# Optimization experiments

Hardware: AMD Instinct MI355X
Metric: run time of the kernel (lower is better)

Reference implementation:

```python
import jax, jax.numpy as jnp
import numpy as np

D_MODEL = 2048
NUM_HEADS = 16
HEAD_DIM = D_MODEL // NUM_HEADS


def setup_inputs() -> dict:
    key = jax.random.key(0)
    ks = jax.random.split(key, 11)
    B, S = 2, 2048
    s = 1.0 / np.sqrt(D_MODEL)
    return {
        "query": jax.random.normal(ks[0], (B, S, D_MODEL), jnp.float32),
        "key_in": jax.random.normal(ks[1], (B, S, D_MODEL), jnp.float32),
        "value": jax.random.normal(ks[2], (B, S, D_MODEL), jnp.float32),
        "Wq": jax.random.normal(ks[3], (D_MODEL, D_MODEL), jnp.float32) * s,
        "bq": jnp.zeros((D_MODEL,), jnp.float32),
        "Wk": jax.random.normal(ks[4], (D_MODEL, D_MODEL), jnp.float32) * s,
        "bk": jnp.zeros((D_MODEL,), jnp.float32),
        "Wv": jax.random.normal(ks[5], (D_MODEL, D_MODEL), jnp.float32) * s,
        "bv": jnp.zeros((D_MODEL,), jnp.float32),
        "Wo": jax.random.normal(ks[6], (D_MODEL, D_MODEL), jnp.float32) * s,
        "bo": jnp.zeros((D_MODEL,), jnp.float32),
    }


def reference(query, key_in, value, Wq, bq, Wk, bk, Wv, bv, Wo, bo):
    B, S, _ = query.shape
    # projections (torch Linear: x @ W.T + b)
    q = query @ Wq.T + bq
    k = key_in @ Wk.T + bk
    v = value @ Wv.T + bv
    # [B, H, S, Dh]
    q = q.reshape(B, S, NUM_HEADS, HEAD_DIM).transpose(0, 2, 1, 3)
    k = k.reshape(B, -1, NUM_HEADS, HEAD_DIM).transpose(0, 2, 1, 3)
    v = v.reshape(B, -1, NUM_HEADS, HEAD_DIM).transpose(0, 2, 1, 3)
    scores = jnp.einsum("bhqd,bhkd->bhqk", q, k) / np.sqrt(HEAD_DIM).astype(np.float32)
    attn = jax.nn.softmax(scores, axis=-1)
    out = jnp.einsum("bhqk,bhkd->bhqd", attn, v)
    out = out.transpose(0, 2, 1, 3).reshape(B, S, D_MODEL)
    return out @ Wo.T + bo
```

## Files before the change

### kernel.cpp

```cpp
#include <hip/hip_runtime.h>
#include <hip/hip_bf16.h>
#include <stdint.h>

typedef __hip_bfloat16 bf16;
typedef __attribute__((ext_vector_type(8))) short bf16x8;
typedef __attribute__((ext_vector_type(4))) float f32x4;
typedef __attribute__((ext_vector_type(4))) short s16x4;

constexpr int D_MODEL   = 2048;
constexpr int NUM_HEADS = 16;
constexpr int HEAD_DIM  = 128;
constexpr int BATCH     = 2;
constexpr int SEQ       = 2048;

constexpr int GBM = 256, GBN = 128, GBK = 64;
constexpr int G_ABUF = GBM * GBK;
constexpr int G_BBUF = GBN * GBK;
constexpr int G_BUF  = G_ABUF + G_BBUF;
constexpr int G_LDS  = 3 * G_BUF;

__device__ __forceinline__ void gload_lds16(const bf16* g, bf16* l) {
    __builtin_amdgcn_global_load_lds(
        (const __attribute__((address_space(1))) void*)g,
        (__attribute__((address_space(3))) void*)l, 16, 0, 0);
}

struct CvtArgs { const float* src[7]; bf16* dst[7]; int n8[7]; };

__global__ __launch_bounds__(256)
void cvt_multi(CvtArgs a)
{
    const int t = blockIdx.y;
    const float* __restrict__ s = a.src[t];
    bf16* __restrict__ d = a.dst[t];
    const int n8 = a.n8[t];
    for (int i = blockIdx.x * 256 + threadIdx.x; i < n8; i += gridDim.x * 256) {
        f32x4 x = *(const f32x4*)(s + (size_t)i * 8);
        f32x4 y = *(const f32x4*)(s + (size_t)i * 8 + 4);
        bf16 t8[8] = { __float2bfloat16(x[0]), __float2bfloat16(x[1]),
                       __float2bfloat16(x[2]), __float2bfloat16(x[3]),
                       __float2bfloat16(y[0]), __float2bfloat16(y[1]),
                       __float2bfloat16(y[2]), __float2bfloat16(y[3]) };
        *(bf16x8*)(d + (size_t)i * 8) = *(const bf16x8*)t8;
    }
}

template <int P>
__device__ __forceinline__
void phase_mfma(f32x4 (&acc)[4][4], bf16x8 (&a)[4][2], bf16x8 (&b)[4][2])
{
#pragma unroll
    for (int kk = 0; kk < 2; kk++) {
#pragma unroll
        for (int j = 0; j <= P; j++)
            acc[P][j] = __builtin_amdgcn_mfma_f32_16x16x32_bf16(a[P][kk], b[j][kk], acc[P][j], 0, 0, 0);
#pragma unroll
        for (int i = 0; i < P; i++)
            acc[i][P] = __builtin_amdgcn_mfma_f32_16x16x32_bf16(a[i][kk], b[P][kk], acc[i][P], 0, 0, 0);
    }
}

template <typename TC, bool TRANS_PERM>
__device__ __forceinline__
void gemm_body(const bf16* __restrict__ A, const bf16* __restrict__ W,
               const float* __restrict__ bias, TC* __restrict__ C,
               int M, int N, int K, bf16* smem)
{
    const int tid  = threadIdx.x;
    const int lane = tid & 63;
    const int wave = tid >> 6;
    const int quad = lane >> 4, l16 = lane & 15;
    const int sw   = l16 & 7;
    const int wr   = wave >> 1;
    const int wc   = wave & 1;
    const int m0   = blockIdx.y * GBM, n0 = blockIdx.x * GBN;

    const int rloc = tid >> 3;
    const int gsw  = (tid & 7) ^ (rloc & 7);
    const int NT   = K / GBK;

    const bf16* Abase = A + (size_t)(m0 + rloc) * K + gsw * 8;
    const bf16* Bbase = W + (size_t)(n0 + rloc) * K + gsw * 8;
    const size_t rstep = (size_t)64 * K;

    auto stageA = [&](int t, int bi, int u) {
        gload_lds16(Abase + u * rstep + (size_t)t * GBK,
                    smem + bi * G_BUF + (u * 512 + tid) * 8);
    };
    auto stageB = [&](int t, int bi, int u) {
        gload_lds16(Bbase + u * rstep + (size_t)t * GBK,
                    smem + bi * G_BUF + G_ABUF + (u * 512 + tid) * 8);
    };

    f32x4 acc[4][4];
#pragma unroll
    for (int i = 0; i < 4; i++)
#pragma unroll
        for (int j = 0; j < 4; j++) acc[i][j] = (f32x4){0.f, 0.f, 0.f, 0.f};

    bf16x8 a[4][2], b[4][2];

#pragma unroll
    for (int u = 0; u < 4; u++) stageA(0, 0, u);
#pragma unroll
    for (int u = 0; u < 2; u++) stageB(0, 0, u);
    if (NT > 1) {
#pragma unroll
        for (int u = 0; u < 4; u++) stageA(1, 1, u);
#pragma unroll
        for (int u = 0; u < 2; u++) stageB(1, 1, u);
        asm volatile("s_waitcnt vmcnt(6)" ::: "memory");
    } else {
        asm volatile("s_waitcnt vmcnt(0)" ::: "memory");
    }
    asm volatile("s_barrier" ::: "memory");

#define GEMM_PHASE(p, STAGE_STMT)                                              \
    {                                                                          \
        STAGE_STMT;                                                            \
        const int rA = wr * 64 + (p) * 16 + l16;                               \
        const int rB = wc * 64 + (p) * 16 + l16;                               \
        a[p][0] = *(const bf16x8*)&sAc[rA * 64 + (quad ^ sw) * 8];             \
        a[p][1] = *(const bf16x8*)&sAc[rA * 64 + (((4 + quad) ^ sw)) * 8];     \
        b[p][0] = *(const bf16x8*)&sBc[rB * 64 + (quad ^ sw) * 8];             \
        b[p][1] = *(const bf16x8*)&sBc[rB * 64 + (((4 + quad) ^ sw)) * 8];     \
        __builtin_amdgcn_s_barrier();                                          \
        __builtin_amdgcn_s_setprio(1);                                         \
        phase_mfma<p>(acc, a, b);                                              \
        __builtin_amdgcn_s_setprio(0);                                         \
    }

    int bc = 0;
    for (int t = 0; t < NT; ++t) {
        const bf16* sAc = smem + bc * G_BUF;
        const bf16* sBc = sAc + G_ABUF;
        const int bs = (bc + 2 >= 3) ? bc - 1 : bc + 2;
        const bool pf = (t + 2 < NT);

        GEMM_PHASE(0, if (pf) { stageA(t + 2, bs, 0); stageA(t + 2, bs, 1); })
        __builtin_amdgcn_s_barrier();
        GEMM_PHASE(1, if (pf) { stageA(t + 2, bs, 2); stageA(t + 2, bs, 3); })
        __builtin_amdgcn_s_barrier();
        GEMM_PHASE(2, if (pf) { stageB(t + 2, bs, 0); })
        __builtin_amdgcn_s_barrier();
        GEMM_PHASE(3, if (pf) { stageB(t + 2, bs, 1); })
        if (pf)                asm volatile("s_waitcnt vmcnt(6)" ::: "memory");
        else if (t + 1 < NT)   asm volatile("s_waitcnt vmcnt(0)" ::: "memory");
        asm volatile("s_barrier" ::: "memory");
        bc = (bc + 1 == 3) ? 0 : bc + 1;
    }
#undef GEMM_PHASE

#pragma unroll
    for (int j = 0; j < 4; j++) {
        const int col = n0 + wc * 64 + j * 16 + l16;
        const float bv = bias[col];
#pragma unroll
        for (int i = 0; i < 4; i++) {
            const int row0 = m0 + wr * 64 + i * 16 + quad * 4;
            if constexpr (TRANS_PERM) {
                int g   = row0 & 63;
                int tau = g >> 4, qh = (g >> 2) & 3;
                int pp  = (tau >> 1) * 32 + qh * 8 + (tau & 1) * 4;
                int sp  = ((row0 & 2047) & ~63) | pp;
                size_t idx = (size_t)(row0 >> 11) * ((size_t)D_MODEL * SEQ)
                           + (size_t)col * SEQ + sp;
                bf16 t4[4];
#pragma unroll
                for (int r = 0; r < 4; r++) t4[r] = __float2bfloat16(acc[i][j][r] + bv);
                *(s16x4*)&C[idx] = *(const s16x4*)t4;
            } else {
#pragma unroll
                for (int r = 0; r < 4; r++) {
                    int row = row0 + r;
                    if constexpr (sizeof(TC) == 2)
                        C[(size_t)row * N + col] = (TC)__float2bfloat16(acc[i][j][r] + bv);
                    else
                        C[(size_t)row * N + col] = (TC)(acc[i][j][r] + bv);
                }
            }
        }
    }
}

template <typename TC, bool TRANS_PERM>
__global__ __launch_bounds__(512, 1)
void gemm_bf16(const bf16* __restrict__ A, const bf16* __restrict__ W,
               const float* __restrict__ bias, TC* __restrict__ C,
               int M, int N, int K)
{
    __shared__ bf16 smem[G_LDS];
    gemm_body<TC, TRANS_PERM>(A, W, bias, C, M, N, K, smem);
}

struct QkvArgs { const bf16* A[3]; const bf16* W[3]; const float* bias[3]; bf16* C[3]; };

__global__ __launch_bounds__(512, 1)
void gemm_qkv(QkvArgs ga, int M, int N, int K)
{
    __shared__ bf16 smem[G_LDS];
    const int z = blockIdx.z;
    if (z == 2) gemm_body<bf16, true >(ga.A[2], ga.W[2], ga.bias[2], ga.C[2], M, N, K, smem);
    else        gemm_body<bf16, false>(ga.A[z], ga.W[z], ga.bias[z], ga.C[z], M, N, K, smem);
}

struct QkArgs { const bf16* A[2]; const bf16* W[2]; const float* bias[2]; bf16* C[2]; };

__global__ __launch_bounds__(512, 1)
void gemm_qk(QkArgs ga, int M, int N, int K)
{
    __shared__ bf16 smem[G_LDS];
    const int z = blockIdx.z;
    gemm_body<bf16, false>(ga.A[z], ga.W[z], ga.bias[z], ga.C[z], M, N, K, smem);
}

__global__ __launch_bounds__(256)
void flash_attn_kernel(const bf16* __restrict__ Qp, const bf16* __restrict__ Kp,
                       const bf16* __restrict__ Vt, bf16* __restrict__ Op)
{
    constexpr int BQ = 128, BKV = 64, DH = 128;
    __shared__ bf16 sK[2][BKV * DH];
    __shared__ bf16 sV[2][DH * BKV];

    const int tid  = threadIdx.x;
    const int wave = tid >> 6, lane = tid & 63;
    const int quad = lane >> 4, l16 = lane & 15;
    const int q0 = blockIdx.x * BQ;
    const int h  = blockIdx.y;
    const int b  = blockIdx.z;

    const size_t base  = (size_t)b * SEQ * D_MODEL + (size_t)h * HEAD_DIM;
    const size_t basev = ((size_t)b * NUM_HEADS + h) * (size_t)HEAD_DIM * SEQ;
    const bf16* Kb = Kp + base;
    const bf16* Vb = Vt + basev;

    auto stage = [&](int t, int bi) {
        const bf16* Kt = Kb + (size_t)t * BKV * D_MODEL;
        const bf16* Vtile = Vb + (size_t)t * BKV;
        bf16* sKb = sK[bi];
        bf16* sVb = sV[bi];
#pragma unroll
        for (int s = 0; s < 4; s++) {
            int c = s * 256 + wave * 64 + lane;
            int row = c >> 4, gs = c & 15;
            int g = gs ^ (row & 15);
            gload_lds16(Kt + (size_t)row * D_MODEL + g * 8, sKb + (size_t)c * 8);
        }
#pragma unroll
        for (int s = 0; s < 4; s++) {
            int c = s * 256 + wave * 64 + lane;
            int dh = c >> 3, gs = c & 7;
            int g = gs ^ (dh & 7);
            gload_lds16(Vtile + (size_t)dh * SEQ + g * 8, sVb + (size_t)c * 8);
        }
    };

    bf16x8 bq[2][4];
#pragma unroll
    for (int nt = 0; nt < 2; nt++)
#pragma unroll
        for (int kk = 0; kk < 4; kk++)
            bq[nt][kk] = *(const bf16x8*)&Qp[base +
                (size_t)(q0 + wave * 32 + nt * 16 + l16) * D_MODEL + kk * 32 + quad * 8];

    f32x4 oacc[2][8];
#pragma unroll
    for (int nt = 0; nt < 2; nt++)
#pragma unroll
        for (int mt = 0; mt < 8; mt++) oacc[nt][mt] = (f32x4){0.f, 0.f, 0.f, 0.f};

    float lsum[2] = {0.f, 0.f};

    const float SCL2E = 0.08838834764831845f * 1.4426950408889634f;
    constexpr int NT = SEQ / BKV;

    stage(0, 0);

    for (int t = 0; t < NT; ++t) {
        __syncthreads();
        if (t + 1 < NT) stage(t + 1, (t + 1) & 1);

        const bf16* sKc = sK[t & 1];
        const bf16* sVc = sV[t & 1];

        f32x4 sacc[2][4];
#pragma unroll
        for (int nt = 0; nt < 2; nt++)
#pragma unroll
            for (int kt = 0; kt < 4; kt++) sacc[nt][kt] = (f32x4){0.f, 0.f, 0.f, 0.f};
#pragma unroll
        for (int kk = 0; kk < 4; kk++) {
            bf16x8 ak[4];
#pragma unroll
            for (int kt = 0; kt < 4; kt++) {
                int row = kt * 16 + l16;
                int g   = (kk * 4 + quad) ^ l16;
                ak[kt] = *(const bf16x8*)&sKc[(size_t)row * DH + g * 8];
            }
#pragma unroll
            for (int nt = 0; nt < 2; nt++)
#pragma unroll
                for (int kt = 0; kt < 4; kt++)
                    sacc[nt][kt] = __builtin_amdgcn_mfma_f32_16x16x32_bf16(ak[kt], bq[nt][kk], sacc[nt][kt], 0, 0, 0);
        }

        bf16x8 pb[2][2];
#pragma unroll
        for (int nt = 0; nt < 2; nt++) {
            bf16 tmp[16];
#pragma unroll
            for (int kt = 0; kt < 4; kt++) {
#pragma unroll
                for (int r = 0; r < 4; r++) {
                    float p = exp2f(fminf(sacc[nt][kt][r] * SCL2E, 60.f));
                    lsum[nt] += p;
                    tmp[(kt >> 1) * 8 + (kt & 1) * 4 + r] = __float2bfloat16(p);
                }
            }
            pb[nt][0] = *(const bf16x8*)&tmp[0];
            pb[nt][1] = *(const bf16x8*)&tmp[8];
        }

#pragma unroll
        for (int c = 0; c < 2; c++) {
#pragma unroll
            for (int mt = 0; mt < 8; mt++) {
                int row = mt * 16 + l16;
                int g   = (c * 4 + quad) ^ (l16 & 7);
                bf16x8 av = *(const bf16x8*)&sVc[(size_t)row * BKV + g * 8];
#pragma unroll
                for (int nt = 0; nt < 2; nt++)
                    oacc[nt][mt] = __builtin_amdgcn_mfma_f32_16x16x32_bf16(av, pb[nt][c], oacc[nt][mt], 0, 0, 0);
            }
        }
    }

#pragma unroll
    for (int nt = 0; nt < 2; nt++) {
        float v = lsum[nt];
        v += __shfl_xor(v, 16);
        v += __shfl_xor(v, 32);
        lsum[nt] = v;
    }

#pragma unroll
    for (int nt = 0; nt < 2; nt++) {
        float inv = 1.f / lsum[nt];
        int row = q0 + wave * 32 + nt * 16 + l16;
#pragma unroll
        for (int mt = 0; mt < 8; mt++) {
            bf16 t4[4];
#pragma unroll
            for (int r = 0; r < 4; r++) t4[r] = __float2bfloat16(oacc[nt][mt][r] * inv);
            *(s16x4*)&Op[base + (size_t)row * D_MODEL + mt * 16 + quad * 4] = *(const s16x4*)t4;
        }
    }
}

extern "C" void kernel_launch(void* const* d_in, const int* in_sizes, int n_in,
                              void* d_out, int out_size, void* d_ws, size_t ws_size,
                              hipStream_t stream)
{
    const float* query  = (const float*)d_in[0];
    const float* key_in = (const float*)d_in[1];
    const float* value  = (const float*)d_in[2];
    const float* Wq = (const float*)d_in[3];
    const float* bq = (const float*)d_in[4];
    const float* Wk = (const float*)d_in[5];
    const float* bk = (const float*)d_in[6];
    const float* Wv = (const float*)d_in[7];
    const float* bv = (const float*)d_in[8];
    const float* Wo = (const float*)d_in[9];
    const float* bo = (const float*)d_in[10];
    float* out = (float*)d_out;

    const int tokens = BATCH * SEQ;
    const size_t nAct = (size_t)tokens * D_MODEL;
    const size_t nW   = (size_t)D_MODEL * D_MODEL;

    const bool fused_qkv = ws_size >= (6 * nAct + 4 * nW) * sizeof(bf16);

    bf16* p = (bf16*)d_ws;
    bf16* qb  = p; p += nAct;
    bf16* kb  = p; p += nAct;
    bf16* vb  = p; p += nAct;
    bf16* wqb = p; p += nW;
    bf16* wkb = p; p += nW;
    bf16* wvb = p; p += nW;
    bf16* wob = p; p += nW;
    bf16* qp  = p; p += nAct;
    bf16* kp  = p; p += nAct;
    bf16* vpT;
    if (fused_qkv) { vpT = p; p += nAct; }
    else           { vpT = qb; }
    bf16* ap = fused_qkv ? qb : kb;

    CvtArgs ca;
    ca.src[0] = query;  ca.dst[0] = qb;  ca.n8[0] = (int)(nAct / 8);
    ca.src[1] = key_in; ca.dst[1] = kb;  ca.n8[1] = (int)(nAct / 8);
    ca.src[2] = value;  ca.dst[2] = vb;  ca.n8[2] = (int)(nAct / 8);
    ca.src[3] = Wq;     ca.dst[3] = wqb; ca.n8[3] = (int)(nW / 8);
    ca.src[4] = Wk;     ca.dst[4] = wkb; ca.n8[4] = (int)(nW / 8);
    ca.src[5] = Wv;     ca.dst[5] = wvb; ca.n8[5] = (int)(nW / 8);
    ca.src[6] = Wo;     ca.dst[6] = wob; ca.n8[6] = (int)(nW / 8);
    cvt_multi<<<dim3(512, 7), 256, 0, stream>>>(ca);

    if (fused_qkv) {
        QkvArgs qa;
        qa.A[0] = qb; qa.W[0] = wqb; qa.bias[0] = bq; qa.C[0] = qp;
        qa.A[1] = kb; qa.W[1] = wkb; qa.bias[1] = bk; qa.C[1] = kp;
        qa.A[2] = vb; qa.W[2] = wvb; qa.bias[2] = bv; qa.C[2] = vpT;
        dim3 g3(D_MODEL / 128, tokens / 256, 3);
        gemm_qkv<<<g3, 512, 0, stream>>>(qa, tokens, D_MODEL, D_MODEL);
    } else {
        QkArgs qa;
        qa.A[0] = qb; qa.W[0] = wqb; qa.bias[0] = bq; qa.C[0] = qp;
        qa.A[1] = kb; qa.W[1] = wkb; qa.bias[1] = bk; qa.C[1] = kp;
        dim3 g2(D_MODEL / 128, tokens / 256, 2);
        gemm_qk<<<g2, 512, 0, stream>>>(qa, tokens, D_MODEL, D_MODEL);
        dim3 gg(D_MODEL / 128, tokens / 256);
        gemm_bf16<bf16, true><<<gg, 512, 0, stream>>>(vb, wvb, bv, vpT, tokens, D_MODEL, D_MODEL);
    }

    dim3 ga(SEQ / 128, NUM_HEADS, BATCH);
    flash_attn_kernel<<<ga, 256, 0, stream>>>(qp, kp, vpT, ap);

    dim3 gg(D_MODEL / 128, tokens / 256);
    gemm_bf16<float, false><<<gg, 512, 0, stream>>>(ap, wob, bo, out, tokens, D_MODEL, D_MODEL);
}
```

Measured before the change: 488.6 us.

## Restructure GEMM main loop with double-buffered register fragments and inline-asm LDS reads

The GEMM inner loop is rewritten so that each K tile issues all its global-to-LDS prefetches at once. It then runs MFMAs on fragments held in registers while the next tile's fragments are read from LDS by a single inline-asm block of ds_read_b128 instructions. Register fragments are ping-ponged across a loop unrolled by two, and the per-phase barriers are removed, leaving one barrier per tile. Launch bounds are also raised to two blocks per CU, which constrains registers and may cause spills, and LDS use (about 144KB per block) may not allow a second block anyway.

```diff
diff --git a/kernel.cpp b/kernel.cpp
--- a/kernel.cpp
+++ b/kernel.cpp
@@ -24,6 +24,8 @@
         (const __attribute__((address_space(1))) void*)g,
         (__attribute__((address_space(3))) void*)l, 16, 0, 0);
 }
+
+typedef __attribute__((address_space(3))) const bf16 lds_cbf16;
 
 struct CvtArgs { const float* src[7]; bf16* dst[7]; int n8[7]; };
 
@@ -45,20 +47,67 @@
     }
 }
 
-template <int P>
-__device__ __forceinline__
-void phase_mfma(f32x4 (&acc)[4][4], bf16x8 (&a)[4][2], bf16x8 (&b)[4][2])
-{
-#pragma unroll
-    for (int kk = 0; kk < 2; kk++) {
-#pragma unroll
-        for (int j = 0; j <= P; j++)
-            acc[P][j] = __builtin_amdgcn_mfma_f32_16x16x32_bf16(a[P][kk], b[j][kk], acc[P][j], 0, 0, 0);
-#pragma unroll
-        for (int i = 0; i < P; i++)
-            acc[i][P] = __builtin_amdgcn_mfma_f32_16x16x32_bf16(a[i][kk], b[P][kk], acc[i][P], 0, 0, 0);
-    }
-}
+
+#define DS_READ16(A0, B0, A1, B1, vA0, vB0, vA1, vB1)                          \
+    asm volatile(                                                              \
+        "ds_read_b128 %0, %16 offset:0\n\t"                                    \
+        "ds_read_b128 %1, %16 offset:2048\n\t"                                 \
+        "ds_read_b128 %2, %16 offset:4096\n\t"                                 \
+        "ds_read_b128 %3, %16 offset:6144\n\t"                                 \
+        "ds_read_b128 %4, %17 offset:0\n\t"                                    \
+        "ds_read_b128 %5, %17 offset:2048\n\t"                                 \
+        "ds_read_b128 %6, %17 offset:4096\n\t"                                 \
+        "ds_read_b128 %7, %17 offset:6144\n\t"                                 \
+        "ds_read_b128 %8, %18 offset:0\n\t"                                    \
+        "ds_read_b128 %9, %18 offset:2048\n\t"                                 \
+        "ds_read_b128 %10, %18 offset:4096\n\t"                                \
+        "ds_read_b128 %11, %18 offset:6144\n\t"                                \
+        "ds_read_b128 %12, %19 offset:0\n\t"                                   \
+        "ds_read_b128 %13, %19 offset:2048\n\t"                                \
+        "ds_read_b128 %14, %19 offset:4096\n\t"                                \
+        "ds_read_b128 %15, %19 offset:6144"                                    \
+        : "=&v"(A0[0]), "=&v"(A0[1]), "=&v"(A0[2]), "=&v"(A0[3]),              \
+          "=&v"(B0[0]), "=&v"(B0[1]), "=&v"(B0[2]), "=&v"(B0[3]),              \
+          "=&v"(A1[0]), "=&v"(A1[1]), "=&v"(A1[2]), "=&v"(A1[3]),              \
+          "=&v"(B1[0]), "=&v"(B1[1]), "=&v"(B1[2]), "=&v"(B1[3])               \
+        : "v"(vA0), "v"(vB0), "v"(vA1), "v"(vB1))
+
+#define MFMA_HALF(AR, BR)                                                      \
+    {                                                                          \
+        __builtin_amdgcn_s_setprio(1);                                         \
+        _Pragma("unroll")                                                      \
+        for (int i_ = 0; i_ < 4; i_++)                                         \
+            _Pragma("unroll")                                                  \
+            for (int j_ = 0; j_ < 4; j_++)                                     \
+                acc[i_][j_] = __builtin_amdgcn_mfma_f32_16x16x32_bf16(         \
+                    AR[i_], BR[j_], acc[i_][j_], 0, 0, 0);                     \
+        __builtin_amdgcn_s_setprio(0);                                         \
+        __builtin_amdgcn_sched_barrier(0);                                     \
+    }
+
+#define GEMM_TILE(t, CA0, CB0, CA1, CB1, NA0, NB0, NA1, NB1)                   \
+    {                                                                          \
+        const int  bs_ = (bc + 2 >= 3) ? bc - 1 : bc + 2;                      \
+        const bool pf_ = (t) + 2 < NT;                                         \
+        if (pf_) { stageA((t) + 2, bs_, 0); stageA((t) + 2, bs_, 1);           \
+                   stageA((t) + 2, bs_, 2); stageA((t) + 2, bs_, 3);           \
+                   stageB((t) + 2, bs_, 0); stageB((t) + 2, bs_, 1); }         \
+        asm volatile("s_waitcnt lgkmcnt(0)" ::: "memory");    \
+        __builtin_amdgcn_sched_barrier(0);                                     \
+        MFMA_HALF(CA0, CB0);                                                   \
+        if (pf_)               asm volatile("s_waitcnt vmcnt(6)" ::: "memory");\
+        else if ((t) + 1 < NT) asm volatile("s_waitcnt vmcnt(0)" ::: "memory");\
+        asm volatile("s_barrier" ::: "memory");          \
+        if ((t) + 1 < NT) {                                                    \
+            const int bn_ = (bc + 1 >= 3) ? 0 : bc + 1;                        \
+            const uint32_t nA_ = aoffTh + (uint32_t)(bn_ * (G_BUF * 2));       \
+            const uint32_t nB_ = boffTh + (uint32_t)(bn_ * (G_BUF * 2));       \
+            DS_READ16(NA0, NB0, NA1, NB1, nA_, nB_, nA_ ^ 64u, nB_ ^ 64u);     \
+            __builtin_amdgcn_sched_barrier(0);        \
+        }                                                                      \
+        MFMA_HALF(CA1, CB1);                                                   \
+        bc = (bc + 1 == 3) ? 0 : bc + 1;                                       \
+    }
 
 template <typename TC, bool TRANS_PERM>
 __device__ __forceinline__
@@ -92,13 +141,19 @@
                     smem + bi * G_BUF + G_ABUF + (u * 512 + tid) * 8);
     };
 
+    const uint32_t aoffTh = (uint32_t)(uintptr_t)(lds_cbf16*)
+        &smem[(wr * 64 + l16) * 64 + (quad ^ sw) * 8];
+    const uint32_t boffTh = (uint32_t)(uintptr_t)(lds_cbf16*)
+        &smem[G_ABUF + (wc * 64 + l16) * 64 + (quad ^ sw) * 8];
+
     f32x4 acc[4][4];
 #pragma unroll
     for (int i = 0; i < 4; i++)
 #pragma unroll
         for (int j = 0; j < 4; j++) acc[i][j] = (f32x4){0.f, 0.f, 0.f, 0.f};
 
-    bf16x8 a[4][2], b[4][2];
+    bf16x8 pa0[4], pb0[4], pa1[4], pb1[4];
+    bf16x8 qa0[4], qb0[4], qa1[4], qb1[4];
 
 #pragma unroll
     for (int u = 0; u < 4; u++) stageA(0, 0, u);
@@ -114,42 +169,14 @@
         asm volatile("s_waitcnt vmcnt(0)" ::: "memory");
     }
     asm volatile("s_barrier" ::: "memory");
-
-#define GEMM_PHASE(p, STAGE_STMT)                                              \
-    {                                                                          \
-        STAGE_STMT;                                                            \
-        const int rA = wr * 64 + (p) * 16 + l16;                               \
-        const int rB = wc * 64 + (p) * 16 + l16;                               \
-        a[p][0] = *(const bf16x8*)&sAc[rA * 64 + (quad ^ sw) * 8];             \
-        a[p][1] = *(const bf16x8*)&sAc[rA * 64 + (((4 + quad) ^ sw)) * 8];     \
-        b[p][0] = *(const bf16x8*)&sBc[rB * 64 + (quad ^ sw) * 8];             \
-        b[p][1] = *(const bf16x8*)&sBc[rB * 64 + (((4 + quad) ^ sw)) * 8];     \
-        __builtin_amdgcn_s_barrier();                                          \
-        __builtin_amdgcn_s_setprio(1);                                         \
-        phase_mfma<p>(acc, a, b);                                              \
-        __builtin_amdgcn_s_setprio(0);                                         \
-    }
+    DS_READ16(pa0, pb0, pa1, pb1, aoffTh, boffTh, aoffTh ^ 64u, boffTh ^ 64u);
+    __builtin_amdgcn_sched_barrier(0);
 
     int bc = 0;
-    for (int t = 0; t < NT; ++t) {
-        const bf16* sAc = smem + bc * G_BUF;
-        const bf16* sBc = sAc + G_ABUF;
-        const int bs = (bc + 2 >= 3) ? bc - 1 : bc + 2;
-        const bool pf = (t + 2 < NT);
-
-        GEMM_PHASE(0, if (pf) { stageA(t + 2, bs, 0); stageA(t + 2, bs, 1); })
-        __builtin_amdgcn_s_barrier();
-        GEMM_PHASE(1, if (pf) { stageA(t + 2, bs, 2); stageA(t + 2, bs, 3); })
-        __builtin_amdgcn_s_barrier();
-        GEMM_PHASE(2, if (pf) { stageB(t + 2, bs, 0); })
-        __builtin_amdgcn_s_barrier();
-        GEMM_PHASE(3, if (pf) { stageB(t + 2, bs, 1); })
-        if (pf)                asm volatile("s_waitcnt vmcnt(6)" ::: "memory");
-        else if (t + 1 < NT)   asm volatile("s_waitcnt vmcnt(0)" ::: "memory");
-        asm volatile("s_barrier" ::: "memory");
-        bc = (bc + 1 == 3) ? 0 : bc + 1;
-    }
-#undef GEMM_PHASE
+    for (int t = 0; t < NT; t += 2) {
+        GEMM_TILE(t,     pa0, pb0, pa1, pb1,  qa0, qb0, qa1, qb1);
+        GEMM_TILE(t + 1, qa0, qb0, qa1, qb1,  pa0, pb0, pa1, pb1);
+    }
 
 #pragma unroll
     for (int j = 0; j < 4; j++) {
@@ -184,7 +211,7 @@
 }
 
 template <typename TC, bool TRANS_PERM>
-__global__ __launch_bounds__(512, 1)
+__global__ __launch_bounds__(512, 2)
 void gemm_bf16(const bf16* __restrict__ A, const bf16* __restrict__ W,
                const float* __restrict__ bias, TC* __restrict__ C,
                int M, int N, int K)
@@ -195,7 +222,7 @@
 
 struct QkvArgs { const bf16* A[3]; const bf16* W[3]; const float* bias[3]; bf16* C[3]; };
 
-__global__ __launch_bounds__(512, 1)
+__global__ __launch_bounds__(512, 2)
 void gemm_qkv(QkvArgs ga, int M, int N, int K)
 {
     __shared__ bf16 smem[G_LDS];
@@ -206,7 +233,7 @@
 
 struct QkArgs { const bf16* A[2]; const bf16* W[2]; const float* bias[2]; bf16* C[2]; };
 
-__global__ __launch_bounds__(512, 1)
+__global__ __launch_bounds__(512, 2)
 void gemm_qk(QkArgs ga, int M, int N, int K)
 {
     __shared__ bf16 smem[G_LDS];
```

Measured after the change: 445.8 us. -8.8%, faster.
